# Kernel optimization log

Measured on AMD Instinct MI355X. Metric: run time of the kernel, lower is better.

Reference implementation:

```python
import jax, jax.numpy as jnp
import numpy as np

BN_EPS = 1e-5


def setup_inputs() -> dict:
    key = jax.random.key(0)
    ks = jax.random.split(key, 7)
    B, C, N = 8, 512, 2048
    P = C // 2
    x = jax.random.normal(ks[0], (B, C, N), dtype=jnp.float32)
    # 1x1 conv weights (no bias), shape [out, in]
    Wg = jax.random.normal(ks[1], (P, C), dtype=jnp.float32) * (1.0 / np.sqrt(C))
    Wtheta = jax.random.normal(ks[2], (P, C), dtype=jnp.float32) * (1.0 / np.sqrt(C))
    Wphi = jax.random.normal(ks[3], (P, C), dtype=jnp.float32) * (1.0 / np.sqrt(C))
    Wz = jax.random.normal(ks[4], (C, P), dtype=jnp.float32) * (1.0 / np.sqrt(P))
    gamma = jnp.ones((C,), dtype=jnp.float32)
    beta = jnp.zeros((C,), dtype=jnp.float32)
    return {"x": x, "Wg": Wg, "Wtheta": Wtheta, "Wphi": Wphi, "Wz": Wz,
            "gamma": gamma, "beta": beta}


def reference(x, Wg, Wtheta, Wphi, Wz, gamma, beta):
    # x: [B, C, N]
    g = jnp.einsum('pc,bcn->bnp', Wg, x)        # [B, N, P]
    theta = jnp.einsum('pc,bcn->bnp', Wtheta, x)  # [B, N, P]
    phi = jnp.einsum('pc,bcn->bpn', Wphi, x)      # [B, P, N]
    f = jnp.einsum('bnp,bpm->bnm', theta, phi)    # [B, N, N] unscaled scores
    f = jax.nn.softmax(f, axis=-1)
    y = jnp.einsum('bnm,bmp->bpn', f, g)          # [B, P, N]
    z = jnp.einsum('cp,bpn->bcn', Wz, y)          # [B, C, N]
    # BatchNorm1d (training-mode batch stats over batch and length dims)
    mean = jnp.mean(z, axis=(0, 2), keepdims=True)
    var = jnp.mean((z - mean) ** 2, axis=(0, 2), keepdims=True)
    z_bn = (z - mean) / jnp.sqrt(var + BN_EPS)
    z_bn = z_bn * gamma[None, :, None] + beta[None, :, None]
    return z_bn + x
```

## Files before the change

### kernel.cpp

```cpp
#include <hip/hip_runtime.h>
#include <hip/hip_bf16.h>


typedef __attribute__((ext_vector_type(8))) short short8;
typedef __attribute__((ext_vector_type(4))) float floatx4;

__device__ __forceinline__ unsigned short f2bf(float v) {
    __hip_bfloat16 h = __float2bfloat16(v);
    return *(unsigned short*)&h;
}
__device__ __forceinline__ float bf2f(unsigned short u) {
    __hip_bfloat16 h;
    *(unsigned short*)&h = u;
    return __bfloat162float(h);
}

__device__ __forceinline__ void gl16(const unsigned short* g, unsigned short* l) {
    __builtin_amdgcn_global_load_lds(
        (const __attribute__((address_space(1))) unsigned int*)g,
        (__attribute__((address_space(3))) unsigned int*)l, 16, 0, 0);
}

__global__ __launch_bounds__(256) void transpose_split(
    const float* __restrict__ X, unsigned short* __restrict__ Thi,
    unsigned short* __restrict__ Tlo, int R, int N)
{
    X   += (long)blockIdx.z * R * N;
    Thi += (long)blockIdx.z * N * R;
    Tlo += (long)blockIdx.z * N * R;
    __shared__ float s[32][33];
    const int tx = threadIdx.x & 31, ty = threadIdx.x >> 5;
    const int n0 = blockIdx.x * 32, r0 = blockIdx.y * 32;
#pragma unroll
    for (int r = 0; r < 4; ++r)
        s[ty + r * 8][tx] = X[(long)(r0 + ty + r * 8) * N + n0 + tx];
    __syncthreads();
#pragma unroll
    for (int r = 0; r < 4; ++r) {
        const int n = ty + r * 8;
        const float v = s[tx][n];
        const unsigned short hi = f2bf(v);
        const unsigned short lo = f2bf(v - bf2f(hi));
        Thi[(long)(n0 + n) * R + r0 + tx] = hi;
        Tlo[(long)(n0 + n) * R + r0 + tx] = lo;
    }
}

__global__ __launch_bounds__(256) void split_w2(
    const float* __restrict__ Wth, const float* __restrict__ Wph,
    unsigned short* __restrict__ Whi, unsigned short* __restrict__ Wlo, int PC)
{
    const int i = blockIdx.x * 256 + threadIdx.x;
    if (i < 2 * PC) {
        const float v = (i < PC) ? Wth[i] : Wph[i - PC];
        const unsigned short hi = f2bf(v);
        Whi[i] = hi;
        Wlo[i] = f2bf(v - bf2f(hi));
    }
}

__global__ __launch_bounds__(256) void cast_bf16(
    const float* __restrict__ X, unsigned short* __restrict__ Y)
{
    const long i = ((long)blockIdx.x * 256 + threadIdx.x) * 4;
    const float4 v = *(const float4*)&X[i];
    ushort4 o;
    o.x = f2bf(v.x); o.y = f2bf(v.y); o.z = f2bf(v.z); o.w = f2bf(v.w);
    *(ushort4*)&Y[i] = o;
}

#define BK 32

template <bool SPLIT, int OUTMODE, int FM, int FN>
__global__ __launch_bounds__(256) void mfma_gemm(
    const unsigned short* __restrict__ Ahi, const unsigned short* __restrict__ Alo,
    const unsigned short* __restrict__ Bhi, const unsigned short* __restrict__ Blo,
    void* __restrict__ Cout, void* __restrict__ Cout2,
    int K, int lda, int ldb, int ldc,
    long sA, long sB, long sC,
    float* __restrict__ S1, float* __restrict__ S2)
{
    constexpr int MTM = FM * 32, MTN = FN * 32;
    constexpr int SA = FM / 2, SB = FN / 2;
    constexpr int ASZ = MTM * BK, BSZ = MTN * BK;

    Ahi += (long)blockIdx.z * sA;
    Bhi += (long)blockIdx.z * sB;
    if (SPLIT) { Alo += (long)blockIdx.z * sA; Blo += (long)blockIdx.z * sB; }
    float* Cf = (float*)Cout + (long)blockIdx.z * sC;
    unsigned short* Ch = (unsigned short*)Cout + (long)blockIdx.z * sC;
    unsigned short* Cl = (unsigned short*)Cout2 + (long)blockIdx.z * sC;

    __shared__ unsigned short AsH[2 * ASZ], BsH[2 * BSZ];
    __shared__ unsigned short AsL[SPLIT ? 2 * ASZ : 8], BsL[SPLIT ? 2 * BSZ : 8];

    const int tid = threadIdx.x;
    const int wid = tid >> 6, lane = tid & 63;
    const int wm = (wid >> 1) * (FM * 16), wn = (wid & 1) * (FN * 16);
    const int l15 = lane & 15, quad = lane >> 4;
    const int m0 = blockIdx.y * MTM, n0 = blockIdx.x * MTN;

    int arow[SA], acol[SA], brow[SB], bcol[SB];
#pragma unroll
    for (int t = 0; t < SA; ++t) {
        const int gid = t * 256 + tid;
        arow[t] = gid >> 2; acol[t] = (gid & 3) * 8;
    }
#pragma unroll
    for (int t = 0; t < SB; ++t) {
        const int gid = t * 256 + tid;
        brow[t] = gid >> 2; bcol[t] = (gid & 3) * 8;
    }

    auto stage = [&](int k0, int buf) {
#pragma unroll
        for (int t = 0; t < SA; ++t) {
            const long o = (long)(m0 + arow[t]) * lda + k0 + acol[t];
            const int d = buf * ASZ + (t * 256 + tid) * 8;
            gl16(&Ahi[o], &AsH[d]);
            if (SPLIT) gl16(&Alo[o], &AsL[d]);
        }
#pragma unroll
        for (int t = 0; t < SB; ++t) {
            const long o = (long)(n0 + brow[t]) * ldb + k0 + bcol[t];
            const int d = buf * BSZ + (t * 256 + tid) * 8;
            gl16(&Bhi[o], &BsH[d]);
            if (SPLIT) gl16(&Blo[o], &BsL[d]);
        }
    };

    floatx4 acc[FM][FN];
#pragma unroll
    for (int i = 0; i < FM; ++i)
#pragma unroll
        for (int j = 0; j < FN; ++j) acc[i][j] = (floatx4){0.f, 0.f, 0.f, 0.f};

    const int iters = K / BK;
    stage(0, 0);
    __syncthreads();

    for (int it = 0; it < iters; ++it) {
        const int cur = it & 1;
        if (it + 1 < iters) stage((it + 1) * BK, cur ^ 1);

        short8 ah[FM], bh[FN], al[SPLIT ? FM : 1], bl[SPLIT ? FN : 1];
#pragma unroll
        for (int i = 0; i < FM; ++i) {
            ah[i] = *(const short8*)&AsH[cur * ASZ + (wm + i * 16 + l15) * BK + quad * 8];
            if (SPLIT) al[i] = *(const short8*)&AsL[cur * ASZ + (wm + i * 16 + l15) * BK + quad * 8];
        }
#pragma unroll
        for (int j = 0; j < FN; ++j) {
            bh[j] = *(const short8*)&BsH[cur * BSZ + (wn + j * 16 + l15) * BK + quad * 8];
            if (SPLIT) bl[j] = *(const short8*)&BsL[cur * BSZ + (wn + j * 16 + l15) * BK + quad * 8];
        }
#pragma unroll
        for (int i = 0; i < FM; ++i)
#pragma unroll
            for (int j = 0; j < FN; ++j) {
                acc[i][j] = __builtin_amdgcn_mfma_f32_16x16x32_bf16(ah[i], bh[j], acc[i][j], 0, 0, 0);
                if (SPLIT) {
                    acc[i][j] = __builtin_amdgcn_mfma_f32_16x16x32_bf16(ah[i], bl[j], acc[i][j], 0, 0, 0);
                    acc[i][j] = __builtin_amdgcn_mfma_f32_16x16x32_bf16(al[i], bh[j], acc[i][j], 0, 0, 0);
                }
            }

        __syncthreads();
    }

#pragma unroll
    for (int i = 0; i < FM; ++i)
#pragma unroll
        for (int j = 0; j < FN; ++j) {
            const int m = m0 + wm + i * 16 + quad * 4;
            const int n = n0 + wn + j * 16 + l15;
#pragma unroll
            for (int r = 0; r < 4; ++r) {
                const float v = acc[i][j][r];
                const long idx = (long)(m + r) * ldc + n;
                if (OUTMODE == 0) {
                    Cf[idx] = v;
                } else if (OUTMODE == 1 || OUTMODE == 3) {
                    Ch[idx] = f2bf(v);
                } else {
                    const unsigned short hi = f2bf(v);
                    Ch[idx] = hi;
                    Cl[idx] = f2bf(v - bf2f(hi));
                }
            }
        }

    if (OUTMODE == 3) {
        const int slot = (blockIdx.z * gridDim.x + blockIdx.x) * 2 + (wn >> 6);
#pragma unroll
        for (int i = 0; i < FM; ++i)
#pragma unroll
            for (int r = 0; r < 4; ++r) {
                float s = 0.f, q = 0.f;
#pragma unroll
                for (int j = 0; j < FN; ++j) {
                    const float v = acc[i][j][r];
                    s += v; q += v * v;
                }
#pragma unroll
                for (int msk = 1; msk < 16; msk <<= 1) {
                    s += __shfl_xor(s, msk, 64);
                    q += __shfl_xor(q, msk, 64);
                }
                if (l15 == 0) {
                    const int row = m0 + wm + i * 16 + quad * 4 + r;
                    S1[(long)row * 256 + slot] = s;
                    S2[(long)row * 256 + slot] = q;
                }
            }
    }
}

#define PSTRP 136

__device__ __forceinline__ int swz64(int row, int slot) {
    return (row << 6) + (((slot ^ row) & 7) << 3);
}

__global__ __launch_bounds__(256, 2) void fused_attn(
    const unsigned short* __restrict__ thphH,
    const unsigned short* __restrict__ thphL,
    const unsigned short* __restrict__ gbf,
    float* __restrict__ yp,
    float2* __restrict__ ml)
{
    const int N = 2048, P = 256, P2 = 512;
    const int id = blockIdx.x;
    const int b  = id & 7;
    const int kh = (id >> 3) & 1;
    const int qt = id >> 4;
    const int q0 = qt * 64;

    const unsigned short* thB = thphH + (long)b * N * P2;
    const unsigned short* tlB = thphL + (long)b * N * P2;
    const unsigned short* gB  = gbf   + (long)b * P * N;
    float*  ypB = yp + (long)kh * (8L * N * P) + (long)b * N * P;
    float2* mlB = ml + (long)kh * (8L * N) + (long)b * N;

    __shared__ unsigned short FG[2 * 128 * 64];
    unsigned short* Fh = FG;
    unsigned short* Fl = FG + 128 * 64;
    unsigned short* Gs = FG;
    __shared__ unsigned short Pw[4][16 * PSTRP];
    __shared__ float Aly[64];

    const int tid = threadIdx.x;
    const int wid = tid >> 6, lane = tid & 63;
    const int l15 = lane & 15, quad = lane >> 4;

    short8 tHr[8], tLr[8];
    {
        const unsigned short* t1 = thB + (long)(q0 + wid * 16 + l15) * P2;
        const unsigned short* t2 = tlB + (long)(q0 + wid * 16 + l15) * P2;
#pragma unroll
        for (int kt = 0; kt < 8; ++kt) {
            tHr[kt] = *(const short8*)&t1[kt * 32 + quad * 8];
            tLr[kt] = *(const short8*)&t2[kt * 32 + quad * 8];
        }
    }

    float mrun[4], lrun[4];
#pragma unroll
    for (int r = 0; r < 4; ++r) { mrun[r] = -1e30f; lrun[r] = 0.f; }

    floatx4 oacc[16];
#pragma unroll
    for (int p = 0; p < 16; ++p) oacc[p] = (floatx4){0.f, 0.f, 0.f, 0.f};

    const int prow4 = tid >> 2, lslot = tid & 3;
    short8 pfH[2][2], pfL[2][2];
    short8 pg[2][4];

    for (int mt = 0; mt < 8; ++mt) {
        const int m0 = kh * 1024 + mt * 128;

        floatx4 sacc[8];
#pragma unroll
        for (int j = 0; j < 8; ++j) sacc[j] = (floatx4){0.f, 0.f, 0.f, 0.f};

#pragma unroll
        for (int s = 0; s < 2; ++s) {
            const long o = (long)(m0 + s * 64 + prow4) * P2 + P + 0 * 32 + lslot * 8;
            pfH[0][s] = *(const short8*)&thB[o];
            pfL[0][s] = *(const short8*)&tlB[o];
        }
#pragma unroll
        for (int s = 0; s < 2; ++s) {
            const int row = s * 64 + prow4;
            *(short8*)&Fh[swz64(row, lslot)] = pfH[0][s];
            *(short8*)&Fl[swz64(row, lslot)] = pfL[0][s];
        }
#pragma unroll
        for (int s = 0; s < 2; ++s) {
            const long o = (long)(m0 + s * 64 + prow4) * P2 + P + 1 * 32 + lslot * 8;
            pfH[1][s] = *(const short8*)&thB[o];
            pfL[1][s] = *(const short8*)&tlB[o];
        }
        __syncthreads();

#pragma unroll
        for (int kc = 0; kc < 8; ++kc) {
            if (kc < 6) {
#pragma unroll
                for (int s = 0; s < 2; ++s) {
                    const long o = (long)(m0 + s * 64 + prow4) * P2 + P + (kc + 2) * 32 + lslot * 8;
                    pfH[kc & 1][s] = *(const short8*)&thB[o];
                    pfL[kc & 1][s] = *(const short8*)&tlB[o];
                }
            }
            const short8 aH = tHr[kc];
            const short8 aL = tLr[kc];
            const int half = (kc & 1) * 4;
            __builtin_amdgcn_s_setprio(1);
#pragma unroll
            for (int j = 0; j < 8; ++j) {
                const int ro = swz64(j * 16 + l15, half + quad);
                const short8 bh = *(const short8*)&Fh[ro];
                const short8 bl = *(const short8*)&Fl[ro];
                sacc[j] = __builtin_amdgcn_mfma_f32_16x16x32_bf16(aH, bh, sacc[j], 0, 0, 0);
                sacc[j] = __builtin_amdgcn_mfma_f32_16x16x32_bf16(aH, bl, sacc[j], 0, 0, 0);
                sacc[j] = __builtin_amdgcn_mfma_f32_16x16x32_bf16(aL, bh, sacc[j], 0, 0, 0);
            }
            __builtin_amdgcn_s_setprio(0);
            if (kc < 7) {
                const int wh = ((kc + 1) & 1) * 4;
#pragma unroll
                for (int s = 0; s < 2; ++s) {
                    const int row = s * 64 + prow4;
                    *(short8*)&Fh[swz64(row, wh + lslot)] = pfH[(kc + 1) & 1][s];
                    *(short8*)&Fl[swz64(row, wh + lslot)] = pfL[(kc + 1) & 1][s];
                }
            }
            __syncthreads();
        }

        float alpha[4];
#pragma unroll
        for (int r = 0; r < 4; ++r) {
            float v = sacc[0][r];
#pragma unroll
            for (int j = 1; j < 8; ++j) v = fmaxf(v, sacc[j][r]);
            v = fmaxf(v, __shfl_xor(v, 1, 64));
            v = fmaxf(v, __shfl_xor(v, 2, 64));
            v = fmaxf(v, __shfl_xor(v, 4, 64));
            v = fmaxf(v, __shfl_xor(v, 8, 64));
            const float mo = mrun[r];
            const float mn = fmaxf(mo, v);
            mrun[r] = mn;
            alpha[r] = __expf(mo - mn);
        }
        float lpart[4] = {0.f, 0.f, 0.f, 0.f};
#pragma unroll
        for (int j = 0; j < 8; ++j)
#pragma unroll
            for (int r = 0; r < 4; ++r) {
                const float p = __expf(sacc[j][r] - mrun[r]);
                Pw[wid][(quad * 4 + r) * PSTRP + j * 16 + l15] = f2bf(p);
                lpart[r] += p;
            }
#pragma unroll
        for (int r = 0; r < 4; ++r) {
            float s = lpart[r];
            s += __shfl_xor(s, 1, 64);
            s += __shfl_xor(s, 2, 64);
            s += __shfl_xor(s, 4, 64);
            s += __shfl_xor(s, 8, 64);
            lrun[r] = lrun[r] * alpha[r] + s;
        }
        if (l15 == 0) {
#pragma unroll
            for (int r = 0; r < 4; ++r) Aly[wid * 16 + quad * 4 + r] = alpha[r];
        }

#pragma unroll
        for (int s = 0; s < 4; ++s)
            pg[0][s] = *(const short8*)&gB[(long)(s * 64 + prow4) * N + m0 + 0 * 32 + lslot * 8];
#pragma unroll
        for (int s = 0; s < 4; ++s)
            *(short8*)&Gs[swz64(s * 64 + prow4, lslot)] = pg[0][s];
#pragma unroll
        for (int s = 0; s < 4; ++s)
            pg[1][s] = *(const short8*)&gB[(long)(s * 64 + prow4) * N + m0 + 1 * 32 + lslot * 8];
        __syncthreads();

        float alr[4][4];
#pragma unroll
        for (int g = 0; g < 4; ++g)
#pragma unroll
            for (int r = 0; r < 4; ++r) alr[g][r] = Aly[g * 16 + quad * 4 + r];
        int noresc = 1;
#pragma unroll
        for (int g = 0; g < 4; ++g)
#pragma unroll
            for (int r = 0; r < 4; ++r) noresc &= (alr[g][r] == 1.f);
        if (!__all(noresc)) {
#pragma unroll
            for (int g = 0; g < 4; ++g)
#pragma unroll
                for (int pj = 0; pj < 4; ++pj)
#pragma unroll
                    for (int r = 0; r < 4; ++r) oacc[g * 4 + pj][r] *= alr[g][r];
        }

#pragma unroll
        for (int mc = 0; mc < 4; ++mc) {
            if (mc < 2) {
#pragma unroll
                for (int s = 0; s < 4; ++s)
                    pg[mc & 1][s] = *(const short8*)&gB[(long)(s * 64 + prow4) * N + m0 + (mc + 2) * 32 + lslot * 8];
            }
            const int half = (mc & 1) * 4;
            short8 af[4];
#pragma unroll
            for (int g = 0; g < 4; ++g)
                af[g] = *(const short8*)&Pw[g][l15 * PSTRP + mc * 32 + quad * 8];
            __builtin_amdgcn_s_setprio(1);
#pragma unroll
            for (int pj = 0; pj < 4; ++pj) {
                const short8 bg = *(const short8*)&Gs[swz64(wid * 64 + pj * 16 + l15, half + quad)];
#pragma unroll
                for (int g = 0; g < 4; ++g)
                    oacc[g * 4 + pj] = __builtin_amdgcn_mfma_f32_16x16x32_bf16(af[g], bg, oacc[g * 4 + pj], 0, 0, 0);
            }
            __builtin_amdgcn_s_setprio(0);
            if (mc < 3) {
                const int wh = ((mc + 1) & 1) * 4;
#pragma unroll
                for (int s = 0; s < 4; ++s)
                    *(short8*)&Gs[swz64(s * 64 + prow4, wh + lslot)] = pg[(mc + 1) & 1][s];
                __syncthreads();
            }
        }
    }

    if (l15 == 0) {
#pragma unroll
        for (int r = 0; r < 4; ++r) Aly[wid * 16 + quad * 4 + r] = 1.0f / lrun[r];
    }
    __syncthreads();
    float liv[4][4];
#pragma unroll
    for (int g = 0; g < 4; ++g)
#pragma unroll
        for (int r = 0; r < 4; ++r) liv[g][r] = Aly[g * 16 + quad * 4 + r];
#pragma unroll
    for (int g = 0; g < 4; ++g)
#pragma unroll
        for (int pj = 0; pj < 4; ++pj)
#pragma unroll
            for (int r = 0; r < 4; ++r) {
                const int row = q0 + g * 16 + quad * 4 + r;
                const int col = wid * 64 + pj * 16 + l15;
                ypB[(long)row * P + col] = oacc[g * 4 + pj][r] * liv[g][r];
            }
    if (l15 == 0) {
#pragma unroll
        for (int r = 0; r < 4; ++r) {
            const int row = q0 + wid * 16 + quad * 4 + r;
            mlB[row] = float2{mrun[r], lrun[r]};
        }
    }
}

__global__ __launch_bounds__(256) void attn_merge(
    const float* __restrict__ yp, const float2* __restrict__ ml,
    unsigned short* __restrict__ ybf)
{
    const long HALF = 8L * 2048 * 256;
    const long t = (long)blockIdx.x * 256 + threadIdx.x;
    const long row = t >> 5;
    const int  c0  = ((int)t & 31) * 8;
    const float2 a = ml[row];
    const float2 c = ml[8L * 2048 + row];
    const float mx = fmaxf(a.x, c.x);
    const float w1 = a.y * __expf(a.x - mx);
    const float w2 = c.y * __expf(c.x - mx);
    const float inv = 1.0f / (w1 + w2);
    const float f1 = w1 * inv, f2 = w2 * inv;
    const long base = row * 256 + c0;
    const float4 u0 = *(const float4*)&yp[base];
    const float4 u1 = *(const float4*)&yp[base + 4];
    const float4 v0 = *(const float4*)&yp[HALF + base];
    const float4 v1 = *(const float4*)&yp[HALF + base + 4];
    ushort4 o0, o1;
    o0.x = f2bf(f1 * u0.x + f2 * v0.x);
    o0.y = f2bf(f1 * u0.y + f2 * v0.y);
    o0.z = f2bf(f1 * u0.z + f2 * v0.z);
    o0.w = f2bf(f1 * u0.w + f2 * v0.w);
    o1.x = f2bf(f1 * u1.x + f2 * v1.x);
    o1.y = f2bf(f1 * u1.y + f2 * v1.y);
    o1.z = f2bf(f1 * u1.z + f2 * v1.z);
    o1.w = f2bf(f1 * u1.w + f2 * v1.w);
    *(ushort4*)&ybf[base] = o0;
    *(ushort4*)&ybf[base + 4] = o1;
}

__global__ __launch_bounds__(256) void bn_finalize(
    const float* __restrict__ p1, const float* __restrict__ p2,
    float* __restrict__ mean, float* __restrict__ rstd, float cnt)
{
    const int c = blockIdx.x, t = threadIdx.x;
    __shared__ float rs[256], rq[256];
    rs[t] = p1[(long)c * 256 + t];
    rq[t] = p2[(long)c * 256 + t];
    __syncthreads();
    for (int st = 128; st > 0; st >>= 1) {
        if (t < st) { rs[t] += rs[t + st]; rq[t] += rq[t + st]; }
        __syncthreads();
    }
    if (t == 0) {
        const float m = rs[0] / cnt;
        mean[c] = m;
        rstd[c] = rsqrtf(rq[0] / cnt - m * m + 1e-5f);
    }
}

__global__ __launch_bounds__(256) void bn_apply_bf(
    const unsigned short* __restrict__ z, const float* __restrict__ x,
    const float* __restrict__ mean, const float* __restrict__ rstd,
    const float* __restrict__ gamma, const float* __restrict__ beta,
    float* __restrict__ out, int C, int N)
{
    const long i = ((long)blockIdx.x * 256 + threadIdx.x) * 8;
    const int c = (int)((i / N) % C);
    const float mu = mean[c], rs = rstd[c], ga = gamma[c], be = beta[c];
    const ushort4 z0 = *(const ushort4*)&z[i];
    const ushort4 z1 = *(const ushort4*)&z[i + 4];
    const float4 x0 = *(const float4*)&x[i];
    const float4 x1 = *(const float4*)&x[i + 4];
    float4 o0, o1;
    o0.x = (bf2f(z0.x) - mu) * rs * ga + be + x0.x;
    o0.y = (bf2f(z0.y) - mu) * rs * ga + be + x0.y;
    o0.z = (bf2f(z0.z) - mu) * rs * ga + be + x0.z;
    o0.w = (bf2f(z0.w) - mu) * rs * ga + be + x0.w;
    o1.x = (bf2f(z1.x) - mu) * rs * ga + be + x1.x;
    o1.y = (bf2f(z1.y) - mu) * rs * ga + be + x1.y;
    o1.z = (bf2f(z1.z) - mu) * rs * ga + be + x1.z;
    o1.w = (bf2f(z1.w) - mu) * rs * ga + be + x1.w;
    *(float4*)&out[i] = o0;
    *(float4*)&out[i + 4] = o1;
}

extern "C" void kernel_launch(void* const* d_in, const int* in_sizes, int n_in,
                              void* d_out, int out_size, void* d_ws, size_t ws_size,
                              hipStream_t stream)
{
    const int B = 8, C = 512, N = 2048, P = 256;
    const float* x      = (const float*)d_in[0];
    const float* Wg     = (const float*)d_in[1];
    const float* Wtheta = (const float*)d_in[2];
    const float* Wphi   = (const float*)d_in[3];
    const float* Wz     = (const float*)d_in[4];
    const float* gamma  = (const float*)d_in[5];
    const float* beta   = (const float*)d_in[6];
    float* out = (float*)d_out;

    float* ws = (float*)d_ws;
    const long NCle = (long)N * C;
    const long NP   = (long)N * P;
    const long R0   = (long)B * NCle;
    unsigned short* xtH   = (unsigned short*)ws;
    unsigned short* xtL   = xtH + B * NCle;
    unsigned short* zbf   = (unsigned short*)ws;
    unsigned short* thphH = (unsigned short*)(ws + R0);
    unsigned short* thphL = thphH + B * NCle;
    unsigned short* gbf   = (unsigned short*)(ws + 2 * R0);
    unsigned short* fbf   = gbf + B * NP;
    unsigned short* ybf   = fbf + (long)B * N * N;
    unsigned short* W2H   = ybf + B * NP;
    unsigned short* W2L   = W2H + 2L * P * C;
    unsigned short* WgB   = W2L + 2L * P * C;
    unsigned short* WzB   = WgB + (long)P * C;
    float*          yp    = (float*)fbf;
    float2*         ml    = (float2*)(ws + 6L * 1024 * 1024);
    float*          bnp1  = ws + R0;
    float*          bnp2  = bnp1 + (long)C * 256;
    float*          mean  = bnp2 + (long)C * 256;
    float*          rstd  = mean + C;

    const long sX = (long)C * N;
    const int  P2 = 2 * P;

    transpose_split<<<dim3(N / 32, C / 32, B), 256, 0, stream>>>(x, xtH, xtL, C, N);
    split_w2<<<(2 * P * C + 255) / 256, 256, 0, stream>>>(Wtheta, Wphi, W2H, W2L, P * C);
    cast_bf16<<<P * C / 1024, 256, 0, stream>>>(Wg, WgB);
    cast_bf16<<<P * C / 1024, 256, 0, stream>>>(Wz, WzB);

    mfma_gemm<true, 2, 4, 4><<<dim3(P2 / 128, N / 128, B), 256, 0, stream>>>(
        xtH, xtL, W2H, W2L, thphH, thphL, C, C, C, P2, NCle, 0, NCle, nullptr, nullptr);
    mfma_gemm<false, 1, 2, 4><<<dim3(N / 128, P / 64, B), 256, 0, stream>>>(
        WgB, WgB, xtH, xtH, gbf, gbf, C, C, C, N, 0, NCle, NP, nullptr, nullptr);

    fused_attn<<<dim3(512), 256, 0, stream>>>(thphH, thphL, gbf, yp, ml);
    attn_merge<<<dim3(2048), 256, 0, stream>>>(yp, ml, ybf);

    mfma_gemm<false, 3, 4, 4><<<dim3(N / 128, C / 128, B), 256, 0, stream>>>(
        WzB, WzB, ybf, ybf, zbf, zbf, P, P, P, N, 0, NP, sX, bnp1, bnp2);

    bn_finalize<<<C, 256, 0, stream>>>(bnp1, bnp2, mean, rstd, (float)B * N);
    bn_apply_bf<<<(int)((B * sX) / 2048), 256, 0, stream>>>(zbf, x, mean, rstd, gamma, beta, out, C, N);
}
```

Measured before the change: 266.9 us.

## Split QK^T across warps by query-half and key-half, stream low theta parts

The score phase is repartitioned. Each warp now handles 32 query rows against 64 of the 128 keys, instead of 16 query rows against all 128 keys, so every B-fragment read from LDS feeds two query tiles. The low-order theta fragments are streamed from global memory per k-chunk rather than held in registers, which reduces register pressure. Row max and row sum now need a cross-warp reduction through shared memory, adding an extra barrier per tile. The P matrix is stored in a single shared buffer indexed by row.

```diff
diff --git a/kernel.cpp b/kernel.cpp
--- a/kernel.cpp
+++ b/kernel.cpp
@@ -246,27 +246,33 @@
     unsigned short* Fh = FG;
     unsigned short* Fl = FG + 128 * 64;
     unsigned short* Gs = FG;
-    __shared__ unsigned short Pw[4][16 * PSTRP];
+    __shared__ unsigned short Pw2[64 * PSTRP];
+    __shared__ float Msh[2][64], Lsh[2][64];
     __shared__ float Aly[64];
 
     const int tid = threadIdx.x;
     const int wid = tid >> 6, lane = tid & 63;
     const int l15 = lane & 15, quad = lane >> 4;
-
-    short8 tHr[8], tLr[8];
-    {
-        const unsigned short* t1 = thB + (long)(q0 + wid * 16 + l15) * P2;
-        const unsigned short* t2 = tlB + (long)(q0 + wid * 16 + l15) * P2;
-#pragma unroll
-        for (int kt = 0; kt < 8; ++kt) {
-            tHr[kt] = *(const short8*)&t1[kt * 32 + quad * 8];
-            tLr[kt] = *(const short8*)&t2[kt * 32 + quad * 8];
-        }
-    }
-
-    float mrun[4], lrun[4];
-#pragma unroll
-    for (int r = 0; r < 4; ++r) { mrun[r] = -1e30f; lrun[r] = 0.f; }
+    const int qh = wid & 1, kv = wid >> 1;
+
+    short8 tHr[2][8];
+#pragma unroll
+    for (int a = 0; a < 2; ++a) {
+        const unsigned short* t = thB + (long)(q0 + qh * 32 + a * 16 + l15) * P2;
+#pragma unroll
+        for (int kc = 0; kc < 8; ++kc)
+            tHr[a][kc] = *(const short8*)&t[kc * 32 + quad * 8];
+    }
+    const unsigned short* tloB[2];
+#pragma unroll
+    for (int a = 0; a < 2; ++a)
+        tloB[a] = tlB + (long)(q0 + qh * 32 + a * 16 + l15) * P2 + quad * 8;
+
+    float mrun[2][4], lrun[2][4];
+#pragma unroll
+    for (int a = 0; a < 2; ++a)
+#pragma unroll
+        for (int r = 0; r < 4; ++r) { mrun[a][r] = -1e30f; lrun[a][r] = 0.f; }
 
     floatx4 oacc[16];
 #pragma unroll
@@ -274,14 +280,17 @@
 
     const int prow4 = tid >> 2, lslot = tid & 3;
     short8 pfH[2][2], pfL[2][2];
+    short8 tLo[2][2];
     short8 pg[2][4];
 
     for (int mt = 0; mt < 8; ++mt) {
         const int m0 = kh * 1024 + mt * 128;
 
-        floatx4 sacc[8];
-#pragma unroll
-        for (int j = 0; j < 8; ++j) sacc[j] = (floatx4){0.f, 0.f, 0.f, 0.f};
+        floatx4 sacc[2][4];
+#pragma unroll
+        for (int a = 0; a < 2; ++a)
+#pragma unroll
+            for (int kt = 0; kt < 4; ++kt) sacc[a][kt] = (floatx4){0.f, 0.f, 0.f, 0.f};
 
 #pragma unroll
         for (int s = 0; s < 2; ++s) {
@@ -301,6 +310,8 @@
             pfH[1][s] = *(const short8*)&thB[o];
             pfL[1][s] = *(const short8*)&tlB[o];
         }
+#pragma unroll
+        for (int a = 0; a < 2; ++a) tLo[0][a] = *(const short8*)&tloB[a][0 * 32];
         __syncthreads();
 
 #pragma unroll
@@ -313,18 +324,24 @@
                     pfL[kc & 1][s] = *(const short8*)&tlB[o];
                 }
             }
-            const short8 aH = tHr[kc];
-            const short8 aL = tLr[kc];
+            if (kc < 7) {
+#pragma unroll
+                for (int a = 0; a < 2; ++a)
+                    tLo[(kc + 1) & 1][a] = *(const short8*)&tloB[a][(kc + 1) * 32];
+            }
             const int half = (kc & 1) * 4;
             __builtin_amdgcn_s_setprio(1);
 #pragma unroll
-            for (int j = 0; j < 8; ++j) {
-                const int ro = swz64(j * 16 + l15, half + quad);
+            for (int kt = 0; kt < 4; ++kt) {
+                const int ro = swz64(kv * 64 + kt * 16 + l15, half + quad);
                 const short8 bh = *(const short8*)&Fh[ro];
                 const short8 bl = *(const short8*)&Fl[ro];
-                sacc[j] = __builtin_amdgcn_mfma_f32_16x16x32_bf16(aH, bh, sacc[j], 0, 0, 0);
-                sacc[j] = __builtin_amdgcn_mfma_f32_16x16x32_bf16(aH, bl, sacc[j], 0, 0, 0);
-                sacc[j] = __builtin_amdgcn_mfma_f32_16x16x32_bf16(aL, bh, sacc[j], 0, 0, 0);
+#pragma unroll
+                for (int a = 0; a < 2; ++a) {
+                    sacc[a][kt] = __builtin_amdgcn_mfma_f32_16x16x32_bf16(tHr[a][kc], bh, sacc[a][kt], 0, 0, 0);
+                    sacc[a][kt] = __builtin_amdgcn_mfma_f32_16x16x32_bf16(tHr[a][kc], bl, sacc[a][kt], 0, 0, 0);
+                    sacc[a][kt] = __builtin_amdgcn_mfma_f32_16x16x32_bf16(tLo[kc & 1][a], bh, sacc[a][kt], 0, 0, 0);
+                }
             }
             __builtin_amdgcn_s_setprio(0);
             if (kc < 7) {
@@ -339,42 +356,65 @@
             __syncthreads();
         }
 
-        float alpha[4];
-#pragma unroll
-        for (int r = 0; r < 4; ++r) {
-            float v = sacc[0][r];
-#pragma unroll
-            for (int j = 1; j < 8; ++j) v = fmaxf(v, sacc[j][r]);
-            v = fmaxf(v, __shfl_xor(v, 1, 64));
-            v = fmaxf(v, __shfl_xor(v, 2, 64));
-            v = fmaxf(v, __shfl_xor(v, 4, 64));
-            v = fmaxf(v, __shfl_xor(v, 8, 64));
-            const float mo = mrun[r];
-            const float mn = fmaxf(mo, v);
-            mrun[r] = mn;
-            alpha[r] = __expf(mo - mn);
-        }
-        float lpart[4] = {0.f, 0.f, 0.f, 0.f};
-#pragma unroll
-        for (int j = 0; j < 8; ++j)
-#pragma unroll
-            for (int r = 0; r < 4; ++r) {
-                const float p = __expf(sacc[j][r] - mrun[r]);
-                Pw[wid][(quad * 4 + r) * PSTRP + j * 16 + l15] = f2bf(p);
-                lpart[r] += p;
-            }
-#pragma unroll
-        for (int r = 0; r < 4; ++r) {
-            float s = lpart[r];
-            s += __shfl_xor(s, 1, 64);
-            s += __shfl_xor(s, 2, 64);
-            s += __shfl_xor(s, 4, 64);
-            s += __shfl_xor(s, 8, 64);
-            lrun[r] = lrun[r] * alpha[r] + s;
-        }
-        if (l15 == 0) {
-#pragma unroll
-            for (int r = 0; r < 4; ++r) Aly[wid * 16 + quad * 4 + r] = alpha[r];
+#pragma unroll
+        for (int a = 0; a < 2; ++a)
+#pragma unroll
+            for (int r = 0; r < 4; ++r) {
+                float v = sacc[a][0][r];
+#pragma unroll
+                for (int kt = 1; kt < 4; ++kt) v = fmaxf(v, sacc[a][kt][r]);
+                v = fmaxf(v, __shfl_xor(v, 1, 64));
+                v = fmaxf(v, __shfl_xor(v, 2, 64));
+                v = fmaxf(v, __shfl_xor(v, 4, 64));
+                v = fmaxf(v, __shfl_xor(v, 8, 64));
+                if (l15 == 0) Msh[kv][qh * 32 + a * 16 + quad * 4 + r] = v;
+            }
+        __syncthreads();
+
+        float alpha[2][4];
+#pragma unroll
+        for (int a = 0; a < 2; ++a)
+#pragma unroll
+            for (int r = 0; r < 4; ++r) {
+                const int row = qh * 32 + a * 16 + quad * 4 + r;
+                const float vm = fmaxf(Msh[0][row], Msh[1][row]);
+                const float mo = mrun[a][r];
+                const float mn = fmaxf(mo, vm);
+                mrun[a][r] = mn;
+                alpha[a][r] = __expf(mo - mn);
+            }
+        float lpart[2][4];
+#pragma unroll
+        for (int a = 0; a < 2; ++a)
+#pragma unroll
+            for (int r = 0; r < 4; ++r) lpart[a][r] = 0.f;
+#pragma unroll
+        for (int a = 0; a < 2; ++a)
+#pragma unroll
+            for (int kt = 0; kt < 4; ++kt)
+#pragma unroll
+                for (int r = 0; r < 4; ++r) {
+                    const float p = __expf(sacc[a][kt][r] - mrun[a][r]);
+                    Pw2[(qh * 32 + a * 16 + quad * 4 + r) * PSTRP + kv * 64 + kt * 16 + l15] = f2bf(p);
+                    lpart[a][r] += p;
+                }
+#pragma unroll
+        for (int a = 0; a < 2; ++a)
+#pragma unroll
+            for (int r = 0; r < 4; ++r) {
+                float s = lpart[a][r];
+                s += __shfl_xor(s, 1, 64);
+                s += __shfl_xor(s, 2, 64);
+                s += __shfl_xor(s, 4, 64);
+                s += __shfl_xor(s, 8, 64);
+                if (l15 == 0) Lsh[kv][qh * 32 + a * 16 + quad * 4 + r] = s;
+            }
+        if (kv == 0 && l15 == 0) {
+#pragma unroll
+            for (int a = 0; a < 2; ++a)
+#pragma unroll
+                for (int r = 0; r < 4; ++r)
+                    Aly[qh * 32 + a * 16 + quad * 4 + r] = alpha[a][r];
         }
 
 #pragma unroll
@@ -388,6 +428,15 @@
             pg[1][s] = *(const short8*)&gB[(long)(s * 64 + prow4) * N + m0 + 1 * 32 + lslot * 8];
         __syncthreads();
 
+#pragma unroll
+        for (int a = 0; a < 2; ++a)
+#pragma unroll
+            for (int r = 0; r < 4; ++r) {
+                const int row = qh * 32 + a * 16 + quad * 4 + r;
+                const float lt = Lsh[0][row] + Lsh[1][row];
+                lrun[a][r] = lrun[a][r] * alpha[a][r] + lt;
+            }
+
         float alr[4][4];
 #pragma unroll
         for (int g = 0; g < 4; ++g)
@@ -418,7 +467,7 @@
             short8 af[4];
 #pragma unroll
             for (int g = 0; g < 4; ++g)
-                af[g] = *(const short8*)&Pw[g][l15 * PSTRP + mc * 32 + quad * 8];
+                af[g] = *(const short8*)&Pw2[(g * 16 + l15) * PSTRP + mc * 32 + quad * 8];
             __builtin_amdgcn_s_setprio(1);
 #pragma unroll
             for (int pj = 0; pj < 4; ++pj) {
@@ -438,9 +487,12 @@
         }
     }
 
-    if (l15 == 0) {
-#pragma unroll
-        for (int r = 0; r < 4; ++r) Aly[wid * 16 + quad * 4 + r] = 1.0f / lrun[r];
+    if (kv == 0 && l15 == 0) {
+#pragma unroll
+        for (int a = 0; a < 2; ++a)
+#pragma unroll
+            for (int r = 0; r < 4; ++r)
+                Aly[qh * 32 + a * 16 + quad * 4 + r] = 1.0f / lrun[a][r];
     }
     __syncthreads();
     float liv[4][4];
@@ -458,12 +510,14 @@
                 const int col = wid * 64 + pj * 16 + l15;
                 ypB[(long)row * P + col] = oacc[g * 4 + pj][r] * liv[g][r];
             }
-    if (l15 == 0) {
-#pragma unroll
-        for (int r = 0; r < 4; ++r) {
-            const int row = q0 + wid * 16 + quad * 4 + r;
-            mlB[row] = float2{mrun[r], lrun[r]};
-        }
+    if (kv == 0 && l15 == 0) {
+#pragma unroll
+        for (int a = 0; a < 2; ++a)
+#pragma unroll
+            for (int r = 0; r < 4; ++r) {
+                const int row = q0 + qh * 32 + a * 16 + quad * 4 + r;
+                mlB[row] = float2{mrun[a][r], lrun[a][r]};
+            }
     }
 }
 
```

Result: slower. 356.0 us (+33.4%).
